# Performance work log

Hardware: AMD Instinct MI355X
Metric: run time of the kernel (lower is better)

The kernel has to match this reference:

```python
import jax, jax.numpy as jnp
import numpy as np

N = 50000        # nodes per type
E = 500000       # edges per relation (~avg degree 10)
D_IN_A, D_IN_B, D_HID, D_OUT, HOP = 256, 128, 128, 64, 2


def setup_inputs():
    key = jax.random.key(0)
    ks = iter(jax.random.split(key, 80))
    nrm = lambda shape, s=0.05: jax.random.normal(next(ks), shape, jnp.float32) * s
    rnd = lambda shape: jax.random.uniform(next(ks), shape, dtype=jnp.float32)
    inp = {"x_A": nrm((N, D_IN_A), 1.0), "x_B": nrm((N, D_IN_B), 1.0)}
    for rel in ("AA", "AB", "BB", "BA"):
        inp["src_" + rel] = jax.random.randint(next(ks), (E,), 0, N)
        inp["dst_" + rel] = jax.random.randint(next(ks), (E,), 0, N)
        inp["val_" + rel] = rnd((E,))
        inp["a2_" + rel] = rnd((N, 1))
    inp["fc1A_w"], inp["fc1A_b"] = nrm((D_IN_A, D_HID)), nrm((D_HID,))
    inp["fc1B_w"], inp["fc1B_b"] = nrm((D_IN_B, D_HID)), nrm((D_HID,))
    for i in range(HOP):
        inp["fcs%d_w" % i], inp["fcs%d_b" % i] = nrm((D_HID, D_HID)), nrm((D_HID,))
        for t in ("A", "B"):
            inp["sa%d%s_w" % (i, t)] = nrm((D_HID, D_HID))
            inp["sa%d%s_b" % (i, t)] = nrm((D_HID,))
            inp["sa%d%s_q" % (i, t)] = nrm((D_HID, 1))
    inp["fc2_w"], inp["fc2_b"] = nrm((D_HID, D_OUT)), nrm((D_OUT,))
    return inp


def _spmm(src, dst, val, x):
    # torch.sparse.mm(A1, x): out[i] = sum_{e: dst[e]==i} val[e] * x[src[e]]
    return jax.ops.segment_sum(val[:, None] * x[src], dst, num_segments=N)


def _sem_att(z, w, b, q):
    # z: (N, M, D); HAN-style semantic attention over the M relations
    s = jnp.tanh(z @ w + b) @ q                         # (N, M, 1)
    beta = jax.nn.softmax(jnp.mean(s, axis=0), axis=0)  # (M, 1)
    return jnp.sum(beta * z, axis=1)                    # (N, D)


def _forward(flt, ints):
    (x_A, x_B, val_AA, a2_AA, val_AB, a2_AB, val_BB, a2_BB, val_BA, a2_BA,
     fc1A_w, fc1A_b, fc1B_w, fc1B_b,
     fcs0_w, fcs0_b, fcs1_w, fcs1_b, fc2_w, fc2_b,
     sa0A_w, sa0A_b, sa0A_q, sa0B_w, sa0B_b, sa0B_q,
     sa1A_w, sa1A_b, sa1A_q, sa1B_w, sa1B_b, sa1B_q) = flt
    (src_AA, dst_AA, src_AB, dst_AB, src_BB, dst_BB, src_BA, dst_BA) = ints
    # fc1 + relu (dropout is identity in eval mode)
    xA = jax.nn.relu(x_A @ fc1A_w + fc1A_b)
    xB = jax.nn.relu(x_B @ fc1B_w + fc1B_b)
    hops = (((fcs0_w, fcs0_b), (sa0A_w, sa0A_b, sa0A_q), (sa0B_w, sa0B_b, sa0B_q)),
            ((fcs1_w, fcs1_b), (sa1A_w, sa1A_b, sa1A_q), (sa1B_w, sa1B_b, sa1B_q)))
    for (fw, fb), saA, saB in hops:
        # shared per-hop linear applied to all node types first
        xA = xA @ fw + fb
        xB = xB @ fw + fb
        # node type A (relations A<-A, A<-B), processed first (dict insertion order)
        hAA = _spmm(src_AA, dst_AA, val_AA, xA) + a2_AA * xA
        hAB = _spmm(src_AB, dst_AB, val_AB, xB) + a2_AB * xA
        xA = jax.nn.relu(_sem_att(jnp.stack((hAA, hAB), axis=1), *saA))
        # node type B sees the already-updated xA (torch mutates dict while iterating)
        hBB = _spmm(src_BB, dst_BB, val_BB, xB) + a2_BB * xB
        hBA = _spmm(src_BA, dst_BA, val_BA, xA) + a2_BA * xB
        xB = jax.nn.relu(_sem_att(jnp.stack((hBB, hBA), axis=1), *saB))
    return xA @ fc2_w + fc2_b  # target_node_type = "A"


def reference(x_A, x_B,
              src_AA, dst_AA, val_AA, a2_AA,
              src_AB, dst_AB, val_AB, a2_AB,
              src_BB, dst_BB, val_BB, a2_BB,
              src_BA, dst_BA, val_BA, a2_BA,
              fc1A_w, fc1A_b, fc1B_w, fc1B_b,
              fcs0_w, fcs0_b, fcs1_w, fcs1_b, fc2_w, fc2_b,
              sa0A_w, sa0A_b, sa0A_q, sa0B_w, sa0B_b, sa0B_q,
              sa1A_w, sa1A_b, sa1A_q, sa1B_w, sa1B_b, sa1B_q):
    flt = (x_A, x_B, val_AA, a2_AA, val_AB, a2_AB, val_BB, a2_BB, val_BA, a2_BA,
           fc1A_w, fc1A_b, fc1B_w, fc1B_b,
           fcs0_w, fcs0_b, fcs1_w, fcs1_b, fc2_w, fc2_b,
           sa0A_w, sa0A_b, sa0A_q, sa0B_w, sa0B_b, sa0B_q,
           sa1A_w, sa1A_b, sa1A_q, sa1B_w, sa1B_b, sa1B_q)
    ints = (src_AA, dst_AA, src_AB, dst_AB, src_BB, dst_BB, src_BA, dst_BA)
    return _forward(flt, ints)
```

## Files before the change

### kernel.cpp

```cpp
#include <hip/hip_runtime.h>
#include <hip/hip_bf16.h>

#define NN 50000
#define NE 500000
#define DH 128
#define INV_N (1.0f / 50000.0f)
#define NBUCK 98
#define BSH 9
#define T1 4096
#define NT1 ((NE + T1 - 1) / T1)
#define GGC 782

using short8 = __attribute__((ext_vector_type(8))) short;
using f32x4 = __attribute__((ext_vector_type(4))) float;
typedef unsigned short u16;

__device__ __forceinline__ float b2f(unsigned short u) {
    unsigned v = (unsigned)u << 16;
    return __builtin_bit_cast(float, v);
}
__device__ __forceinline__ unsigned short f2b(float f) {
    return __builtin_bit_cast(unsigned short, __float2bfloat16(f));
}

struct EdgePtrs {
    const int* src[4];
    const int* dst[4];
    const float* val[4];
};


__global__ void k_bhist(EdgePtrs ep, int* __restrict__ btot) {
    int r = blockIdx.y;
    const int* dst = ep.dst[r];
    __shared__ int h[NBUCK];
    int t = threadIdx.x;
    if (t < NBUCK) h[t] = 0;
    __syncthreads();
    int e0 = blockIdx.x * T1;
#pragma unroll
    for (int i = 0; i < T1 / 256; ++i) {
        int e = e0 + i * 256 + t;
        if (e < NE) atomicAdd(&h[dst[e] >> BSH], 1);
    }
    __syncthreads();
    if (t < NBUCK && h[t] > 0) atomicAdd(&btot[r * NBUCK + t], h[t]);
}

__global__ void k_bscan(const int* __restrict__ btot, int* __restrict__ bbase,
                        int* __restrict__ bcur) {
    __shared__ int s[128];
    int t = threadIdx.x;
    for (int r = 0; r < 4; ++r) {
        int v = (t < NBUCK) ? btot[r * NBUCK + t] : 0;
        if (t < 128) s[t] = v;
        __syncthreads();
        for (int off = 1; off < 128; off <<= 1) {
            int u = (t >= off && t < 128) ? s[t - off] : 0;
            __syncthreads();
            if (t < 128) s[t] += u;
            __syncthreads();
        }
        if (t < NBUCK) {
            int ex = s[t] - v;
            bbase[r * NBUCK + t] = ex;
            bcur[r * NBUCK + t] = ex;
        }
        __syncthreads();
    }
}

__global__ __launch_bounds__(256) void k_msplit(EdgePtrs ep, int* __restrict__ bcur,
                                                int2* __restrict__ esb) {
    int r = blockIdx.y;
    const int* src = ep.src[r];
    const int* dst = ep.dst[r];
    const float* val = ep.val[r];
    __shared__ int2 eb[T1];
    __shared__ int hist[128], lofs[128], lcur[128], sc[128], gbase[NBUCK];
    int t = threadIdx.x;
    int e0 = blockIdx.x * T1;
    int total = NE - e0;
    if (total > T1) total = T1;

    int sreg[T1 / 256], dreg[T1 / 256];
    float vreg[T1 / 256];
#pragma unroll
    for (int i = 0; i < T1 / 256; ++i) {
        int e = e0 + i * 256 + t;
        bool ok = e < NE;
        sreg[i] = ok ? src[e] : 0;
        dreg[i] = ok ? dst[e] : -1;
        vreg[i] = ok ? val[e] : 0.f;
    }
    if (t < 128) { hist[t] = 0; lcur[t] = 0; }
    __syncthreads();
#pragma unroll
    for (int i = 0; i < T1 / 256; ++i)
        if (dreg[i] >= 0) atomicAdd(&hist[dreg[i] >> BSH], 1);
    __syncthreads();
    if (t < 128) sc[t] = hist[t];
    __syncthreads();
    for (int off = 1; off < 128; off <<= 1) {
        int u = (t >= off && t < 128) ? sc[t - off] : 0;
        __syncthreads();
        if (t < 128) sc[t] += u;
        __syncthreads();
    }
    if (t < 128) lofs[t] = sc[t] - hist[t];
    __syncthreads();
#pragma unroll
    for (int i = 0; i < T1 / 256; ++i) {
        if (dreg[i] >= 0) {
            int b = dreg[i] >> BSH;
            int pos = lofs[b] + atomicAdd(&lcur[b], 1);
            eb[pos] = make_int2((int)(((unsigned)dreg[i] << 16) | (unsigned)sreg[i]),
                                __float_as_int(vreg[i]));
        }
    }
    __syncthreads();
    if (t < NBUCK && hist[t] > 0) gbase[t] = atomicAdd(&bcur[r * NBUCK + t], hist[t]);
    __syncthreads();
    for (int j = t; j < total; j += 256) {
        int2 rec = eb[j];
        int b = (int)((unsigned)rec.x >> (16 + BSH));
        esb[(size_t)r * NE + gbase[b] + (j - lofs[b])] = rec;
    }
}

__global__ __launch_bounds__(256) void k_blocal(const int2* __restrict__ esb,
                                                const int* __restrict__ btot,
                                                const int* __restrict__ bbase,
                                                int* __restrict__ rs4,
                                                int2* __restrict__ es4) {
    int r = blockIdx.y, b = blockIdx.x;
    int base = bbase[r * NBUCK + b];
    int cnt = btot[r * NBUCK + b];
    int d0 = b << BSH;
    int dlim = NN - d0;
    if (dlim > (1 << BSH)) dlim = 1 << BSH;
    __shared__ int h[512], pr[512], cur[512], ps[256];
    int t = threadIdx.x;
    h[t] = 0; h[t + 256] = 0;
    cur[t] = 0; cur[t + 256] = 0;
    __syncthreads();
    const int2* ein = esb + (size_t)r * NE + base;
    for (int j = t; j < cnt; j += 256)
        atomicAdd(&h[(int)((unsigned)ein[j].x >> 16) - d0], 1);
    __syncthreads();
    int a0 = h[2 * t], a1 = h[2 * t + 1];
    ps[t] = a0 + a1;
    __syncthreads();
    for (int off = 1; off < 256; off <<= 1) {
        int u = (t >= off) ? ps[t - off] : 0;
        __syncthreads();
        ps[t] += u;
        __syncthreads();
    }
    int ex = ps[t] - (a0 + a1);
    pr[2 * t] = ex;
    pr[2 * t + 1] = ex + a0;
    __syncthreads();
    for (int dl = t; dl < dlim; dl += 256) rs4[r * (NN + 1) + d0 + dl] = base + pr[dl];
    if (b == NBUCK - 1 && t == 0) rs4[r * (NN + 1) + NN] = NE;
    for (int j = t; j < cnt; j += 256) {
        int2 rec = ein[j];
        int dl = (int)((unsigned)rec.x >> 16) - d0;
        int k = atomicAdd(&cur[dl], 1);
        es4[(size_t)r * NE + base + pr[dl] + k] = make_int2(rec.x & 0xFFFF, rec.y);
    }
}


__global__ void k_f2b(const float* __restrict__ src, u16* __restrict__ dst, int n4) {
    int i = blockIdx.x * 256 + threadIdx.x;
    if (i >= n4) return;
    float4 v = ((const float4*)src)[i];
    unsigned lo = (unsigned)f2b(v.x) | ((unsigned)f2b(v.y) << 16);
    unsigned hi = (unsigned)f2b(v.z) | ((unsigned)f2b(v.w) << 16);
    ((uint2*)dst)[i] = make_uint2(lo, hi);
}


struct WDesc { const float* src; u16* dst; int K; int N; int start; };
struct WPack { WDesc d[9]; };

__global__ void k_wt(WPack p) {
    int gid = blockIdx.x * 256 + threadIdx.x;
#pragma unroll
    for (int i = 0; i < 9; ++i) {
        int K = p.d[i].K, N = p.d[i].N;
        int local = gid - p.d[i].start;
        if (local >= 0 && local < K * N) {
            int k = local / N;
            int n = local - k * N;
            float w = p.d[i].src[local];
            unsigned byte = ((unsigned)(n * K + k) * 2u) ^ ((unsigned)(n & 7) << 4);
            *(u16*)((char*)p.d[i].dst + byte) = f2b(w);
            return;
        }
    }
}

template <int KT, int NF, int MODE, bool OUTF32>
__global__ __launch_bounds__(256) void k_mm(const u16* __restrict__ X0, const u16* __restrict__ X1,
                                            int M, const u16* __restrict__ WT,
                                            const float* __restrict__ Bias,
                                            const float* __restrict__ Q,
                                            void* __restrict__ O0, void* __restrict__ O1,
                                            float* __restrict__ S0, float* __restrict__ S1) {
    constexpr int K = KT * 32;
    constexpr int N = NF * 16;
    const u16* X = blockIdx.y ? X1 : X0;
    void* OutV = blockIdx.y ? O1 : O0;
    float* Sout = blockIdx.y ? S1 : S0;

    __shared__ u16 wlds[K * N];
    int t = threadIdx.x;
    constexpr int CH = K * N * 2 / 16;
    const uint4* wg = (const uint4*)WT;
    uint4* wl = (uint4*)wlds;
#pragma unroll
    for (int i = 0; i < CH / 256; ++i) wl[t + i * 256] = wg[t + i * 256];

    int l = t & 63, w = t >> 6;
    int m0 = blockIdx.x * 64 + w * 16;
    int arow = m0 + (l & 15);
    if (arow >= M) arow = M - 1;
    int kh = (l >> 4) * 8;

    short8 a[KT];
    const u16* xp = X + (size_t)arow * K + kh;
#pragma unroll
    for (int kt = 0; kt < KT; ++kt) a[kt] = *(const short8*)(xp + kt * 32);

    __syncthreads();

    f32x4 acc[NF];
#pragma unroll
    for (int i = 0; i < NF; ++i) acc[i] = (f32x4){0.f, 0.f, 0.f, 0.f};

    unsigned sw = (unsigned)((l & 7) << 4);
#pragma unroll
    for (int nf = 0; nf < NF; ++nf) {
        unsigned base = (unsigned)((nf * 16 + (l & 15)) * K) * 2u;
#pragma unroll
        for (int kt = 0; kt < KT; ++kt) {
            unsigned byte = (base + (unsigned)(kt * 32 + kh) * 2u) ^ sw;
            short8 b = *(const short8*)((const char*)wlds + byte);
            acc[nf] = __builtin_amdgcn_mfma_f32_16x16x32_bf16(a[kt], b, acc[nf], 0, 0, 0);
        }
    }

    int col0 = l & 15;
    int rbase = m0 + (l >> 4) * 4;
    if (MODE == 2) {
        float tot = 0.f;
#pragma unroll
        for (int nf = 0; nf < NF; ++nf) {
            int c = nf * 16 + col0;
            float bv = Bias[c], qv = Q[c];
#pragma unroll
            for (int r = 0; r < 4; ++r)
                if (rbase + r < M) tot += tanhf(acc[nf][r] + bv) * qv;
        }
#pragma unroll
        for (int m = 1; m < 64; m <<= 1) tot += __shfl_xor(tot, m);
        __shared__ float wred[4];
        if (l == 0) wred[w] = tot;
        __syncthreads();
        if (t == 0) Sout[blockIdx.x] = wred[0] + wred[1] + wred[2] + wred[3];
    } else {
#pragma unroll
        for (int nf = 0; nf < NF; ++nf) {
            int c = nf * 16 + col0;
            float bv = Bias[c];
#pragma unroll
            for (int r = 0; r < 4; ++r) {
                int row = rbase + r;
                if (row >= M) continue;
                float v = acc[nf][r] + bv;
                if (MODE == 1) v = fmaxf(v, 0.f);
                if (OUTF32)
                    ((float*)OutV)[(size_t)row * N + c] = v;
                else
                    ((u16*)OutV)[(size_t)row * N + c] = f2b(v);
            }
        }
    }
}

struct SpmmDArgs {
    const int* rsA; const int2* esA; const u16* XsA;
    const int* rsB; const int2* esB; const u16* XsB;
    const u16* Xd; const float* a2A; const float* a2B;
    u16* out1; u16* out2;
};

__device__ __forceinline__ void gacc(const u16* __restrict__ Xs, int lane, int2 pe,
                                     float& ax, float& ay) {
    unsigned xv = *(const unsigned*)&Xs[(size_t)pe.x * DH + lane * 2];
    float v = __int_as_float(pe.y);
    ax += v * b2f((u16)xv);
    ay += v * b2f((u16)(xv >> 16));
}

__global__ __launch_bounds__(256) void k_spmmD(SpmmDArgs p) {
    int row = blockIdx.x * 4 + (threadIdx.x >> 6);
    if (row >= NN) return;
    int lane = threadIdx.x & 63;
    unsigned xd = *(const unsigned*)&p.Xd[(size_t)row * DH + lane * 2];
    float xdx = b2f((u16)xd), xdy = b2f((u16)(xd >> 16));
    float aA = p.a2A[row], aB = p.a2B[row];
    float a1x = aA * xdx, a1y = aA * xdy;
    float a2x = aB * xdx, a2y = aB * xdy;
    int eA = p.rsA[row], eAe = p.rsA[row + 1];
    int eB = p.rsB[row], eBe = p.rsB[row + 1];

    while (eA + 4 <= eAe && eB + 4 <= eBe) {
        int2 pa0 = p.esA[eA], pa1 = p.esA[eA + 1], pa2 = p.esA[eA + 2], pa3 = p.esA[eA + 3];
        int2 pb0 = p.esB[eB], pb1 = p.esB[eB + 1], pb2 = p.esB[eB + 2], pb3 = p.esB[eB + 3];
        unsigned xa0 = *(const unsigned*)&p.XsA[(size_t)pa0.x * DH + lane * 2];
        unsigned xa1 = *(const unsigned*)&p.XsA[(size_t)pa1.x * DH + lane * 2];
        unsigned xa2 = *(const unsigned*)&p.XsA[(size_t)pa2.x * DH + lane * 2];
        unsigned xa3 = *(const unsigned*)&p.XsA[(size_t)pa3.x * DH + lane * 2];
        unsigned xb0 = *(const unsigned*)&p.XsB[(size_t)pb0.x * DH + lane * 2];
        unsigned xb1 = *(const unsigned*)&p.XsB[(size_t)pb1.x * DH + lane * 2];
        unsigned xb2 = *(const unsigned*)&p.XsB[(size_t)pb2.x * DH + lane * 2];
        unsigned xb3 = *(const unsigned*)&p.XsB[(size_t)pb3.x * DH + lane * 2];
        float va0 = __int_as_float(pa0.y), va1 = __int_as_float(pa1.y);
        float va2 = __int_as_float(pa2.y), va3 = __int_as_float(pa3.y);
        float vb0 = __int_as_float(pb0.y), vb1 = __int_as_float(pb1.y);
        float vb2 = __int_as_float(pb2.y), vb3 = __int_as_float(pb3.y);
        a1x += va0 * b2f((u16)xa0); a1y += va0 * b2f((u16)(xa0 >> 16));
        a1x += va1 * b2f((u16)xa1); a1y += va1 * b2f((u16)(xa1 >> 16));
        a1x += va2 * b2f((u16)xa2); a1y += va2 * b2f((u16)(xa2 >> 16));
        a1x += va3 * b2f((u16)xa3); a1y += va3 * b2f((u16)(xa3 >> 16));
        a2x += vb0 * b2f((u16)xb0); a2y += vb0 * b2f((u16)(xb0 >> 16));
        a2x += vb1 * b2f((u16)xb1); a2y += vb1 * b2f((u16)(xb1 >> 16));
        a2x += vb2 * b2f((u16)xb2); a2y += vb2 * b2f((u16)(xb2 >> 16));
        a2x += vb3 * b2f((u16)xb3); a2y += vb3 * b2f((u16)(xb3 >> 16));
        eA += 4; eB += 4;
    }
    for (; eA + 4 <= eAe; eA += 4) {
        int2 q0 = p.esA[eA], q1 = p.esA[eA + 1], q2 = p.esA[eA + 2], q3 = p.esA[eA + 3];
        gacc(p.XsA, lane, q0, a1x, a1y);
        gacc(p.XsA, lane, q1, a1x, a1y);
        gacc(p.XsA, lane, q2, a1x, a1y);
        gacc(p.XsA, lane, q3, a1x, a1y);
    }
    for (; eA < eAe; ++eA) gacc(p.XsA, lane, p.esA[eA], a1x, a1y);
    for (; eB + 4 <= eBe; eB += 4) {
        int2 q0 = p.esB[eB], q1 = p.esB[eB + 1], q2 = p.esB[eB + 2], q3 = p.esB[eB + 3];
        gacc(p.XsB, lane, q0, a2x, a2y);
        gacc(p.XsB, lane, q1, a2x, a2y);
        gacc(p.XsB, lane, q2, a2x, a2y);
        gacc(p.XsB, lane, q3, a2x, a2y);
    }
    for (; eB < eBe; ++eB) gacc(p.XsB, lane, p.esB[eB], a2x, a2y);

    unsigned o1 = (unsigned)f2b(a1x) | ((unsigned)f2b(a1y) << 16);
    unsigned o2 = (unsigned)f2b(a2x) | ((unsigned)f2b(a2y) << 16);
    *(unsigned*)&p.out1[(size_t)row * DH + lane * 2] = o1;
    *(unsigned*)&p.out2[(size_t)row * DH + lane * 2] = o2;
}


__global__ void k_combine(const u16* __restrict__ h1, const u16* __restrict__ h2,
                          const float* __restrict__ sp, u16* __restrict__ out, int n8) {
    int t = threadIdx.x;
    float p0 = 0.f, p1 = 0.f;
    for (int j = t; j < GGC; j += 256) {
        p0 += sp[j];
        p1 += sp[GGC + j];
    }
#pragma unroll
    for (int m = 1; m < 64; m <<= 1) {
        p0 += __shfl_xor(p0, m);
        p1 += __shfl_xor(p1, m);
    }
    __shared__ float r0[4], r1[4];
    if ((t & 63) == 0) {
        r0[t >> 6] = p0;
        r1[t >> 6] = p1;
    }
    __syncthreads();
    float s0 = (r0[0] + r0[1] + r0[2] + r0[3]) * INV_N;
    float s1 = (r1[0] + r1[1] + r1[2] + r1[3]) * INV_N;
    float mx = fmaxf(s0, s1);
    float ea = __expf(s0 - mx), eb = __expf(s1 - mx);
    float inv = 1.0f / (ea + eb);
    float b0 = ea * inv, b1 = eb * inv;

    int i = blockIdx.x * 256 + t;
    if (i >= n8) return;
    short8 A = ((const short8*)h1)[i];
    short8 B = ((const short8*)h2)[i];
    short8 O;
#pragma unroll
    for (int j = 0; j < 8; ++j) {
        float v = b0 * b2f((u16)A[j]) + b1 * b2f((u16)B[j]);
        O[j] = (short)f2b(fmaxf(v, 0.f));
    }
    ((short8*)out)[i] = O;
}


extern "C" void kernel_launch(void* const* d_in, const int* in_sizes, int n_in, void* d_out,
                              int out_size, void* d_ws, size_t ws_size, hipStream_t stream) {
    (void)in_sizes; (void)n_in; (void)out_size; (void)ws_size;

    const float* x_A = (const float*)d_in[0];
    const float* x_B = (const float*)d_in[1];
    EdgePtrs ep;
    const float* a2I[4];
    for (int r = 0; r < 4; ++r) {
        ep.src[r] = (const int*)d_in[2 + r * 4];
        ep.dst[r] = (const int*)d_in[3 + r * 4];
        ep.val[r] = (const float*)d_in[4 + r * 4];
        a2I[r] = (const float*)d_in[5 + r * 4];
    }
    const float* fc1A_w = (const float*)d_in[18];
    const float* fc1A_b = (const float*)d_in[19];
    const float* fc1B_w = (const float*)d_in[20];
    const float* fc1B_b = (const float*)d_in[21];
    const float* fcs_w[2] = {(const float*)d_in[22], (const float*)d_in[30]};
    const float* fcs_b[2] = {(const float*)d_in[23], (const float*)d_in[31]};
    const float* saA_w[2] = {(const float*)d_in[24], (const float*)d_in[32]};
    const float* saA_b[2] = {(const float*)d_in[25], (const float*)d_in[33]};
    const float* saA_q[2] = {(const float*)d_in[26], (const float*)d_in[34]};
    const float* saB_w[2] = {(const float*)d_in[27], (const float*)d_in[35]};
    const float* saB_b[2] = {(const float*)d_in[28], (const float*)d_in[36]};
    const float* saB_q[2] = {(const float*)d_in[29], (const float*)d_in[37]};
    const float* fc2_w = (const float*)d_in[38];
    const float* fc2_b = (const float*)d_in[39];

    char* p = (char*)d_ws;
    auto take = [&](size_t bytes) -> void* {
        void* r = (void*)p;
        p += (bytes + 255) & ~(size_t)255;
        return r;
    };
    const size_t NF = (size_t)NN * DH;
    u16* xAbf = (u16*)take((size_t)NN * 256 * 2);
    u16* xBbf = (u16*)take((size_t)NN * 128 * 2);
    u16* xA0 = (u16*)take(NF * 2);
    u16* xA1 = (u16*)take(NF * 2);
    u16* xB0 = (u16*)take(NF * 2);
    u16* xB1 = (u16*)take(NF * 2);
    u16* h1 = (u16*)take(NF * 2);
    u16* h2 = (u16*)take(NF * 2);
    u16* wt_fc1A = (u16*)take(256 * 128 * 2);
    u16* wt_fc1B = (u16*)take(128 * 128 * 2);
    u16* wt_fcs[2] = {(u16*)take(128 * 128 * 2), (u16*)take(128 * 128 * 2)};
    u16* wt_saA[2] = {(u16*)take(128 * 128 * 2), (u16*)take(128 * 128 * 2)};
    u16* wt_saB[2] = {(u16*)take(128 * 128 * 2), (u16*)take(128 * 128 * 2)};
    u16* wt_fc2 = (u16*)take(128 * 64 * 2);
    int* rs4 = (int*)take((size_t)(NN + 1) * 4 * 4);
    int2* es4 = (int2*)take((size_t)NE * 4 * 8);
    int2* esb = (int2*)take((size_t)NE * 4 * 8);
    int* btot = (int*)take(NBUCK * 4 * 4);
    int* bbase = (int*)take(NBUCK * 4 * 4);
    int* bcur = (int*)take(NBUCK * 4 * 4);
    float* spart[4];
    for (int i = 0; i < 4; ++i) spart[i] = (float*)take(2 * GGC * 4);

    const int GG = GGC;
    const int GP = (NN + 3) / 4;
    const int GC8 = (int)(NF / 8 / 256);

    const int* rsR[4];
    const int2* esR[4];
    for (int r = 0; r < 4; ++r) {
        rsR[r] = rs4 + r * (NN + 1);
        esR[r] = es4 + (size_t)r * NE;
    }

    hipMemsetAsync(btot, 0, NBUCK * 4 * 4, stream);
    k_bhist<<<dim3(NT1, 4), 256, 0, stream>>>(ep, btot);
    k_bscan<<<1, 256, 0, stream>>>(btot, bbase, bcur);
    k_msplit<<<dim3(NT1, 4), 256, 0, stream>>>(ep, bcur, esb);
    k_blocal<<<dim3(NBUCK, 4), 256, 0, stream>>>(esb, btot, bbase, rs4, es4);

    k_f2b<<<(NN * 256 / 4 + 255) / 256, 256, 0, stream>>>(x_A, xAbf, NN * 256 / 4);
    k_f2b<<<(NN * 128 / 4 + 255) / 256, 256, 0, stream>>>(x_B, xBbf, NN * 128 / 4);
    {
        WPack wp;
        const float* srcs_[9] = {fc1A_w, fc1B_w, fcs_w[0], fcs_w[1], saA_w[0],
                                 saA_w[1], saB_w[0], saB_w[1], fc2_w};
        u16* dsts_[9] = {wt_fc1A, wt_fc1B, wt_fcs[0], wt_fcs[1], wt_saA[0],
                         wt_saA[1], wt_saB[0], wt_saB[1], wt_fc2};
        int Ks[9] = {256, 128, 128, 128, 128, 128, 128, 128, 128};
        int Ns[9] = {128, 128, 128, 128, 128, 128, 128, 128, 64};
        int start = 0;
        for (int i = 0; i < 9; ++i) {
            wp.d[i] = {srcs_[i], dsts_[i], Ks[i], Ns[i], start};
            start += Ks[i] * Ns[i];
        }
        k_wt<<<(start + 255) / 256, 256, 0, stream>>>(wp);
    }

    k_mm<8, 8, 1, false><<<dim3(GG, 1), 256, 0, stream>>>(xAbf, xAbf, NN, wt_fc1A, fc1A_b,
                                                          nullptr, xA0, xA0, nullptr, nullptr);
    k_mm<4, 8, 1, false><<<dim3(GG, 1), 256, 0, stream>>>(xBbf, xBbf, NN, wt_fc1B, fc1B_b,
                                                          nullptr, xB0, xB0, nullptr, nullptr);

    for (int h = 0; h < 2; ++h) {
        k_mm<4, 8, 0, false><<<dim3(GG, 2), 256, 0, stream>>>(xA0, xB0, NN, wt_fcs[h], fcs_b[h],
                                                              nullptr, xA1, xB1, nullptr, nullptr);
        {
            SpmmDArgs sa = {rsR[0], esR[0], xA1, rsR[1], esR[1], xB1,
                            xA1, a2I[0], a2I[1], h1, h2};
            k_spmmD<<<GP, 256, 0, stream>>>(sa);
        }
        k_mm<4, 8, 2, false><<<dim3(GG, 2), 256, 0, stream>>>(h1, h2, NN, wt_saA[h], saA_b[h],
                                                              saA_q[h], nullptr, nullptr,
                                                              spart[h * 2 + 0],
                                                              spart[h * 2 + 0] + GGC);
        k_combine<<<GC8, 256, 0, stream>>>(h1, h2, spart[h * 2 + 0], xA0, (int)(NF / 8));
        {
            SpmmDArgs sb = {rsR[2], esR[2], xB1, rsR[3], esR[3], xA0,
                            xB1, a2I[2], a2I[3], h1, h2};
            k_spmmD<<<GP, 256, 0, stream>>>(sb);
        }
        k_mm<4, 8, 2, false><<<dim3(GG, 2), 256, 0, stream>>>(h1, h2, NN, wt_saB[h], saB_b[h],
                                                              saB_q[h], nullptr, nullptr,
                                                              spart[h * 2 + 1],
                                                              spart[h * 2 + 1] + GGC);
        k_combine<<<GC8, 256, 0, stream>>>(h1, h2, spart[h * 2 + 1], xB0, (int)(NF / 8));
    }

    k_mm<4, 4, 0, true><<<dim3(GG, 1), 256, 0, stream>>>(xA0, xA0, NN, wt_fc2, fc2_b, nullptr,
                                                         d_out, d_out, nullptr, nullptr);
}
```

Measured before the change: 621.0 us.

## Split SpMM wavefront into four edge groups with 16-byte gathers

Restructures the dual-relation SpMM kernel so each 64-lane wavefront works as four 16-lane groups, each processing a different edge and gathering a full 256-byte bf16 row with 16-byte loads per lane. Partial sums are reduced across groups with cross-lane shuffles, and the next edge's index/value is prefetched one step ahead. This replaces the 4-byte-per-lane gathers with wider loads and more edges in flight, targeting gather latency and load-instruction count. In exchange it adds 16 accumulator registers, a shuffle reduction, and branch divergence when the two relations have different degrees.

Result: slower. 645.9 us (+4.0%).

```diff
diff --git a/kernel.cpp b/kernel.cpp
--- a/kernel.cpp
+++ b/kernel.cpp
@@ -297,72 +297,77 @@
     u16* out1; u16* out2;
 };
 
-__device__ __forceinline__ void gacc(const u16* __restrict__ Xs, int lane, int2 pe,
-                                     float& ax, float& ay) {
-    unsigned xv = *(const unsigned*)&Xs[(size_t)pe.x * DH + lane * 2];
-    float v = __int_as_float(pe.y);
-    ax += v * b2f((u16)xv);
-    ay += v * b2f((u16)(xv >> 16));
+__device__ __forceinline__ void acc8(float* a, uint4 x, float v) {
+    unsigned d0 = x.x, d1 = x.y, d2 = x.z, d3 = x.w;
+    a[0] += v * b2f((u16)d0); a[1] += v * b2f((u16)(d0 >> 16));
+    a[2] += v * b2f((u16)d1); a[3] += v * b2f((u16)(d1 >> 16));
+    a[4] += v * b2f((u16)d2); a[5] += v * b2f((u16)(d2 >> 16));
+    a[6] += v * b2f((u16)d3); a[7] += v * b2f((u16)(d3 >> 16));
 }
 
 __global__ __launch_bounds__(256) void k_spmmD(SpmmDArgs p) {
     int row = blockIdx.x * 4 + (threadIdx.x >> 6);
     if (row >= NN) return;
-    int lane = threadIdx.x & 63;
-    unsigned xd = *(const unsigned*)&p.Xd[(size_t)row * DH + lane * 2];
-    float xdx = b2f((u16)xd), xdy = b2f((u16)(xd >> 16));
-    float aA = p.a2A[row], aB = p.a2B[row];
-    float a1x = aA * xdx, a1y = aA * xdy;
-    float a2x = aB * xdx, a2y = aB * xdy;
+    int l = threadIdx.x & 63;
+    int q = l >> 4, j = l & 15;
+
+    uint4 xd4 = *(const uint4*)&p.Xd[(size_t)row * DH + j * 8];
+    float accA[8], accB[8];
+#pragma unroll
+    for (int c = 0; c < 8; ++c) { accA[c] = 0.f; accB[c] = 0.f; }
+    if (q == 0) {
+        float aA = p.a2A[row];
+        acc8(accA, xd4, aA);
+    } else if (q == 1) {
+        float aB = p.a2B[row];
+        acc8(accB, xd4, aB);
+    }
+
     int eA = p.rsA[row], eAe = p.rsA[row + 1];
     int eB = p.rsB[row], eBe = p.rsB[row + 1];
-
-    while (eA + 4 <= eAe && eB + 4 <= eBe) {
-        int2 pa0 = p.esA[eA], pa1 = p.esA[eA + 1], pa2 = p.esA[eA + 2], pa3 = p.esA[eA + 3];
-        int2 pb0 = p.esB[eB], pb1 = p.esB[eB + 1], pb2 = p.esB[eB + 2], pb3 = p.esB[eB + 3];
-        unsigned xa0 = *(const unsigned*)&p.XsA[(size_t)pa0.x * DH + lane * 2];
-        unsigned xa1 = *(const unsigned*)&p.XsA[(size_t)pa1.x * DH + lane * 2];
-        unsigned xa2 = *(const unsigned*)&p.XsA[(size_t)pa2.x * DH + lane * 2];
-        unsigned xa3 = *(const unsigned*)&p.XsA[(size_t)pa3.x * DH + lane * 2];
-        unsigned xb0 = *(const unsigned*)&p.XsB[(size_t)pb0.x * DH + lane * 2];
-        unsigned xb1 = *(const unsigned*)&p.XsB[(size_t)pb1.x * DH + lane * 2];
-        unsigned xb2 = *(const unsigned*)&p.XsB[(size_t)pb2.x * DH + lane * 2];
-        unsigned xb3 = *(const unsigned*)&p.XsB[(size_t)pb3.x * DH + lane * 2];
-        float va0 = __int_as_float(pa0.y), va1 = __int_as_float(pa1.y);
-        float va2 = __int_as_float(pa2.y), va3 = __int_as_float(pa3.y);
-        float vb0 = __int_as_float(pb0.y), vb1 = __int_as_float(pb1.y);
-        float vb2 = __int_as_float(pb2.y), vb3 = __int_as_float(pb3.y);
-        a1x += va0 * b2f((u16)xa0); a1y += va0 * b2f((u16)(xa0 >> 16));
-        a1x += va1 * b2f((u16)xa1); a1y += va1 * b2f((u16)(xa1 >> 16));
-        a1x += va2 * b2f((u16)xa2); a1y += va2 * b2f((u16)(xa2 >> 16));
-        a1x += va3 * b2f((u16)xa3); a1y += va3 * b2f((u16)(xa3 >> 16));
-        a2x += vb0 * b2f((u16)xb0); a2y += vb0 * b2f((u16)(xb0 >> 16));
-        a2x += vb1 * b2f((u16)xb1); a2y += vb1 * b2f((u16)(xb1 >> 16));
-        a2x += vb2 * b2f((u16)xb2); a2y += vb2 * b2f((u16)(xb2 >> 16));
-        a2x += vb3 * b2f((u16)xb3); a2y += vb3 * b2f((u16)(xb3 >> 16));
-        eA += 4; eB += 4;
-    }
-    for (; eA + 4 <= eAe; eA += 4) {
-        int2 q0 = p.esA[eA], q1 = p.esA[eA + 1], q2 = p.esA[eA + 2], q3 = p.esA[eA + 3];
-        gacc(p.XsA, lane, q0, a1x, a1y);
-        gacc(p.XsA, lane, q1, a1x, a1y);
-        gacc(p.XsA, lane, q2, a1x, a1y);
-        gacc(p.XsA, lane, q3, a1x, a1y);
-    }
-    for (; eA < eAe; ++eA) gacc(p.XsA, lane, p.esA[eA], a1x, a1y);
-    for (; eB + 4 <= eBe; eB += 4) {
-        int2 q0 = p.esB[eB], q1 = p.esB[eB + 1], q2 = p.esB[eB + 2], q3 = p.esB[eB + 3];
-        gacc(p.XsB, lane, q0, a2x, a2y);
-        gacc(p.XsB, lane, q1, a2x, a2y);
-        gacc(p.XsB, lane, q2, a2x, a2y);
-        gacc(p.XsB, lane, q3, a2x, a2y);
-    }
-    for (; eB < eBe; ++eB) gacc(p.XsB, lane, p.esB[eB], a2x, a2y);
-
-    unsigned o1 = (unsigned)f2b(a1x) | ((unsigned)f2b(a1y) << 16);
-    unsigned o2 = (unsigned)f2b(a2x) | ((unsigned)f2b(a2y) << 16);
-    *(unsigned*)&p.out1[(size_t)row * DH + lane * 2] = o1;
-    *(unsigned*)&p.out2[(size_t)row * DH + lane * 2] = o2;
+    const int2 z2 = make_int2(0, 0);
+    int2 rA = (eA + q < eAe) ? p.esA[eA + q] : z2;
+    int2 rB = (eB + q < eBe) ? p.esB[eB + q] : z2;
+
+    while (eA < eAe || eB < eBe) {
+        bool doA = eA < eAe, doB = eB < eBe;
+        int2 cA = rA, cB = rB;
+        int nA = eA + 4, nB = eB + 4;
+        rA = (doA && nA + q < eAe) ? p.esA[nA + q] : z2;
+        rB = (doB && nB + q < eBe) ? p.esB[nB + q] : z2;
+        if (doA) {
+            uint4 x4 = *(const uint4*)&p.XsA[(size_t)cA.x * DH + j * 8];
+            acc8(accA, x4, __int_as_float(cA.y));
+            eA = nA;
+        }
+        if (doB) {
+            uint4 x4 = *(const uint4*)&p.XsB[(size_t)cB.x * DH + j * 8];
+            acc8(accB, x4, __int_as_float(cB.y));
+            eB = nB;
+        }
+    }
+
+#pragma unroll
+    for (int c = 0; c < 8; ++c) {
+        accA[c] += __shfl_xor(accA[c], 16);
+        accA[c] += __shfl_xor(accA[c], 32);
+        accB[c] += __shfl_xor(accB[c], 16);
+        accB[c] += __shfl_xor(accB[c], 32);
+    }
+
+    if (q == 0) {
+        uint4 o1, o2;
+        o1.x = (unsigned)f2b(accA[0]) | ((unsigned)f2b(accA[1]) << 16);
+        o1.y = (unsigned)f2b(accA[2]) | ((unsigned)f2b(accA[3]) << 16);
+        o1.z = (unsigned)f2b(accA[4]) | ((unsigned)f2b(accA[5]) << 16);
+        o1.w = (unsigned)f2b(accA[6]) | ((unsigned)f2b(accA[7]) << 16);
+        o2.x = (unsigned)f2b(accB[0]) | ((unsigned)f2b(accB[1]) << 16);
+        o2.y = (unsigned)f2b(accB[2]) | ((unsigned)f2b(accB[3]) << 16);
+        o2.z = (unsigned)f2b(accB[4]) | ((unsigned)f2b(accB[5]) << 16);
+        o2.w = (unsigned)f2b(accB[6]) | ((unsigned)f2b(accB[7]) << 16);
+        *(uint4*)&p.out1[(size_t)row * DH + j * 8] = o1;
+        *(uint4*)&p.out2[(size_t)row * DH + j * 8] = o2;
+    }
 }
 
 
```
